# Optimization experiments

Measured on AMD Instinct MI355X. Metric: run time of the kernel, lower is better.

## Reference

```python
import jax, jax.numpy as jnp
import numpy as np


def setup_inputs() -> dict:
    key = jax.random.key(0)
    k1, k2, k3 = jax.random.split(key, 3)
    B, N_h, size_in = 128, 512, 1024
    bound = 1.0 / np.sqrt(size_in)
    x = jax.random.normal(k1, (B, size_in), dtype=jnp.float32)
    weights = jax.random.uniform(k2, (N_h, size_in), minval=-bound, maxval=bound, dtype=jnp.float32)
    bias = jax.random.uniform(k3, (N_h,), minval=-bound, maxval=bound, dtype=jnp.float32)
    return {"x": x, "weights": weights, "bias": bias}


def reference(x, weights, bias):
    # Original: out[k,i,l] = sum_{j<l} weights[i,j] * x[k,j] + bias[i]
    # Implemented as an exclusive cumulative sum over the last axis instead of
    # materializing the [B, size_in, size_in] repeat+triu tensor.
    t = x[:, None, :] * weights[None, :, :]          # [B, N_h, size_in]
    c = jnp.cumsum(t, axis=-1)                       # inclusive prefix sum over j
    out = c - t + bias[None, :, None]                # exclusive prefix + bias
    return out
```

## Files before the change

### kernel.cpp

```cpp
#include <hip/hip_runtime.h>


#define SIZE_IN 1024
#define N_H 512

typedef float f32x4 __attribute__((ext_vector_type(4)));

template <int CTRL, int ROW_MASK>
__device__ __forceinline__ float dpp_add(float x) {
    int moved = __builtin_amdgcn_update_dpp(0, __float_as_int(x), CTRL,
                                            ROW_MASK, 0xf, true);
    return x + __int_as_float(moved);
}

__device__ __forceinline__ float wave_incl_scan(float x) {
    x = dpp_add<0x111, 0xf>(x);
    x = dpp_add<0x112, 0xf>(x);
    x = dpp_add<0x114, 0xf>(x);
    x = dpp_add<0x118, 0xf>(x);
    x = dpp_add<0x142, 0xa>(x);
    x = dpp_add<0x143, 0xc>(x);
    return x;
}

__global__ __launch_bounds__(256) void nade_kernel(
    const float* __restrict__ x,
    const float* __restrict__ w,
    const float* __restrict__ bias,
    float* __restrict__ out)
{
    const int lane = threadIdx.x & 63;
    const int wave = threadIdx.x >> 6;
    const int row  = blockIdx.x * 4 + wave;
    const int k = row >> 9;
    const int i = row & (N_H - 1);

    const float* xr = x + (size_t)k * SIZE_IN;
    const float* wr = w + (size_t)i * SIZE_IN;
    float* outr = out + (size_t)row * SIZE_IN;

    float carry = bias[i];
#pragma unroll
    for (int c = 0; c < 4; ++c) {
        const int j0 = c * 256 + lane * 4;
        const f32x4 xv = *reinterpret_cast<const f32x4*>(xr + j0);
        const f32x4 wv = *reinterpret_cast<const f32x4*>(wr + j0);
        const float p0 = xv.x * wv.x;
        const float p1 = p0 + xv.y * wv.y;
        const float p2 = p1 + xv.z * wv.z;
        const float p3 = p2 + xv.w * wv.w;
        const float s = wave_incl_scan(p3);
        const float excl = carry + (s - p3);
        f32x4 ov;
        ov.x = excl;
        ov.y = excl + p0;
        ov.z = excl + p1;
        ov.w = excl + p2;
        *reinterpret_cast<f32x4*>(outr + j0) = ov;
        carry += __int_as_float(__builtin_amdgcn_readlane(__float_as_int(s), 63));
    }
}

extern "C" void kernel_launch(void* const* d_in, const int* in_sizes, int n_in,
                              void* d_out, int out_size, void* d_ws, size_t ws_size,
                              hipStream_t stream) {
    const float* x    = (const float*)d_in[0];
    const float* w    = (const float*)d_in[1];
    const float* bias = (const float*)d_in[2];
    float* out = (float*)d_out;

    const int B = in_sizes[0] / SIZE_IN;
    const int rows = B * N_H;
    const int blocks = rows / 4;

    nade_kernel<<<blocks, 256, 0, stream>>>(x, w, bias, out);
}
```

Baseline: 45.13 us.

## Process four batch rows per wave to reuse weight loads and interleave scans

Each wave now handles one weight row across four batch rows, so a single weight vector load is reused four times. The four independent DPP prefix scans are interleaved step by step, which exposes instruction-level parallelism and hides DPP latency. The grid shrinks by four and each thread holds more registers and issues four output stores per chunk. The kernel is dominated by writing the 256 MB output, so the benefit may be limited.

```diff
diff --git a/kernel.cpp b/kernel.cpp
--- a/kernel.cpp
+++ b/kernel.cpp
@@ -13,16 +13,6 @@
     return x + __int_as_float(moved);
 }
 
-__device__ __forceinline__ float wave_incl_scan(float x) {
-    x = dpp_add<0x111, 0xf>(x);
-    x = dpp_add<0x112, 0xf>(x);
-    x = dpp_add<0x114, 0xf>(x);
-    x = dpp_add<0x118, 0xf>(x);
-    x = dpp_add<0x142, 0xa>(x);
-    x = dpp_add<0x143, 0xc>(x);
-    return x;
-}
-
 __global__ __launch_bounds__(256) void nade_kernel(
     const float* __restrict__ x,
     const float* __restrict__ w,
@@ -31,33 +21,58 @@
 {
     const int lane = threadIdx.x & 63;
     const int wave = threadIdx.x >> 6;
-    const int row  = blockIdx.x * 4 + wave;
-    const int k = row >> 9;
-    const int i = row & (N_H - 1);
+    const int ib = blockIdx.x & 127;
+    const int kb = blockIdx.x >> 7;
+    const int i  = ib * 4 + wave;
+    const int k0 = kb * 4;
 
-    const float* xr = x + (size_t)k * SIZE_IN;
     const float* wr = w + (size_t)i * SIZE_IN;
-    float* outr = out + (size_t)row * SIZE_IN;
+    const float* xr = x + (size_t)k0 * SIZE_IN;
+    float* outr = out + (size_t)(k0 * N_H + i) * SIZE_IN;
+    const float b = bias[i];
 
-    float carry = bias[i];
+    float carry[4] = {b, b, b, b};
 #pragma unroll
     for (int c = 0; c < 4; ++c) {
         const int j0 = c * 256 + lane * 4;
-        const f32x4 xv = *reinterpret_cast<const f32x4*>(xr + j0);
         const f32x4 wv = *reinterpret_cast<const f32x4*>(wr + j0);
-        const float p0 = xv.x * wv.x;
-        const float p1 = p0 + xv.y * wv.y;
-        const float p2 = p1 + xv.z * wv.z;
-        const float p3 = p2 + xv.w * wv.w;
-        const float s = wave_incl_scan(p3);
-        const float excl = carry + (s - p3);
-        f32x4 ov;
-        ov.x = excl;
-        ov.y = excl + p0;
-        ov.z = excl + p1;
-        ov.w = excl + p2;
-        *reinterpret_cast<f32x4*>(outr + j0) = ov;
-        carry += __int_as_float(__builtin_amdgcn_readlane(__float_as_int(s), 63));
+
+        float p0[4], p1[4], p2[4], p3[4], s[4];
+#pragma unroll
+        for (int r = 0; r < 4; ++r) {
+            const f32x4 xv = *reinterpret_cast<const f32x4*>(xr + r * SIZE_IN + j0);
+            p0[r] = xv.x * wv.x;
+            p1[r] = p0[r] + xv.y * wv.y;
+            p2[r] = p1[r] + xv.z * wv.z;
+            p3[r] = p2[r] + xv.w * wv.w;
+            s[r]  = p3[r];
+        }
+
+#pragma unroll
+        for (int r = 0; r < 4; ++r) s[r] = dpp_add<0x111, 0xf>(s[r]);
+#pragma unroll
+        for (int r = 0; r < 4; ++r) s[r] = dpp_add<0x112, 0xf>(s[r]);
+#pragma unroll
+        for (int r = 0; r < 4; ++r) s[r] = dpp_add<0x114, 0xf>(s[r]);
+#pragma unroll
+        for (int r = 0; r < 4; ++r) s[r] = dpp_add<0x118, 0xf>(s[r]);
+#pragma unroll
+        for (int r = 0; r < 4; ++r) s[r] = dpp_add<0x142, 0xa>(s[r]);
+#pragma unroll
+        for (int r = 0; r < 4; ++r) s[r] = dpp_add<0x143, 0xc>(s[r]);
+
+#pragma unroll
+        for (int r = 0; r < 4; ++r) {
+            const float excl = carry[r] + (s[r] - p3[r]);
+            f32x4 ov;
+            ov.x = excl;
+            ov.y = excl + p0[r];
+            ov.z = excl + p1[r];
+            ov.w = excl + p2[r];
+            *reinterpret_cast<f32x4*>(outr + (size_t)r * (N_H * SIZE_IN) + j0) = ov;
+            carry[r] += __int_as_float(
+                __builtin_amdgcn_readlane(__float_as_int(s[r]), 63));
+        }
     }
 }
 
@@ -70,8 +85,6 @@
     float* out = (float*)d_out;
 
     const int B = in_sizes[0] / SIZE_IN;
-    const int rows = B * N_H;
-    const int blocks = rows / 4;
-
+    const int blocks = (B / 4) * (N_H / 4);
     nade_kernel<<<blocks, 256, 0, stream>>>(x, w, bias, out);
 }
```

Result: slower. 49.26 us (+9.2%).
